# Optimization experiments

Hardware: AMD Instinct MI355X
Metric: run time of the kernel (lower is better)

The kernel has to match this reference:

```python
import jax, jax.numpy as jnp
import numpy as np

N, IN_DIM, HEADS, C = 100000, 128, 4, 32  # out_dim = HEADS*C = 128
E = 1600000


def setup_inputs() -> dict:
    key = jax.random.key(0)
    ks = jax.random.split(key, 9)
    x = jax.random.normal(ks[0], (N, IN_DIM), dtype=jnp.float32)
    edge_index = jax.random.randint(ks[1], (2, E), 0, N, dtype=jnp.int64)
    # GATConv params
    W = jax.random.normal(ks[2], (HEADS * C, IN_DIM), dtype=jnp.float32) * (1.0 / np.sqrt(IN_DIM))
    att_src = jax.random.normal(ks[3], (HEADS, C), dtype=jnp.float32) * 0.1
    att_dst = jax.random.normal(ks[4], (HEADS, C), dtype=jnp.float32) * 0.1
    bias = jax.random.normal(ks[5], (HEADS * C,), dtype=jnp.float32) * 0.01
    # complex phase + LayerNorm params
    phase = jax.random.normal(ks[6], (HEADS * C,), dtype=jnp.float32) * 0.02
    gamma = 1.0 + jax.random.normal(ks[7], (HEADS * C,), dtype=jnp.float32) * 0.01
    beta = jax.random.normal(ks[8], (HEADS * C,), dtype=jnp.float32) * 0.01
    return {"x": x, "edge_index": edge_index, "W": W, "att_src": att_src,
            "att_dst": att_dst, "bias": bias, "phase": phase, "gamma": gamma, "beta": beta}


def reference(x, edge_index, W, att_src, att_dst, bias, phase, gamma, beta):
    src, dst = edge_index[0], edge_index[1]
    h = (x @ W.T).reshape(N, HEADS, C)                      # [N,H,C]
    a_src = jnp.einsum('nhc,hc->nh', h, att_src)            # [N,H]
    a_dst = jnp.einsum('nhc,hc->nh', h, att_dst)
    e = jax.nn.leaky_relu(a_src[src] + a_dst[dst], 0.2)     # [E,H]
    # segment softmax over destination nodes (numerically stable)
    m = jax.ops.segment_max(e, dst, num_segments=N)         # [N,H]
    ex = jnp.exp(e - m[dst])
    s = jax.ops.segment_sum(ex, dst, num_segments=N)        # [N,H]
    alpha = ex / (s[dst] + 1e-16)                           # [E,H]
    msg = h[src] * alpha[:, :, None]                        # [E,H,C]
    out = jax.ops.segment_sum(msg, dst, num_segments=N).reshape(N, HEADS * C) + bias
    # complex phase magnitude: sqrt((h cos p)^2 + (h sin p)^2 + eps)
    mag = jnp.sqrt((out * jnp.cos(phase)) ** 2 + (out * jnp.sin(phase)) ** 2 + 1e-12)
    # LayerNorm
    mu = mag.mean(-1, keepdims=True)
    var = ((mag - mu) ** 2).mean(-1, keepdims=True)
    hn = (mag - mu) / jnp.sqrt(var + 1e-5) * gamma + beta
    return jax.nn.gelu(hn, approximate=False)
```

## Files before the change

kernel.cpp:

```cpp
#include <hip/hip_runtime.h>
#include <hip/hip_bf16.h>

#define N_ 100000
#define E_ 1600000
#define D_ 128
#define H_ 4
#define C_ 32
#define CAP 64
#define XSTR 136
#define NBUILD 256
#define NLIN 512

using bf16 = __hip_bfloat16;
typedef __attribute__((ext_vector_type(8))) short short8;
typedef __attribute__((ext_vector_type(4))) float f32x4;
typedef __attribute__((ext_vector_type(2))) float f32x2;

__device__ __forceinline__ float u2f(unsigned u) { return __uint_as_float(u); }
__device__ __forceinline__ unsigned short f2bu(float v) {
  bf16 t = __float2bfloat16(v);
  return *(unsigned short*)&t;
}

__global__ __launch_bounds__(256) void k_build_linear(
    const float* __restrict__ x, const float* __restrict__ W,
    const float* __restrict__ att_src, const float* __restrict__ att_dst,
    const int* __restrict__ ei, int* __restrict__ cnt, int* __restrict__ slot,
    bf16* __restrict__ h, float* __restrict__ a_src, float* __restrict__ a_dst) {
  __shared__ unsigned short WB[16384];
  __shared__ unsigned short XS[64 * XSTR];
  __shared__ float ats[128], atd[128];
  const int tid = threadIdx.x;
  const int bid = blockIdx.x;
  const int role = bid % 3;

  if (role == 0) {
    const int bb = bid / 3;
    for (int base = bb * 1024; base < E_; base += NBUILD * 1024) {
      const int e0 = base + tid;
      const int e1 = base + 256 + tid;
      const int e2 = base + 512 + tid;
      const int e3 = base + 768 + tid;
      int d0 = 0, d1 = 0, d2 = 0, d3 = 0, s0 = 0, s1 = 0, s2 = 0, s3 = 0;
      if (e0 < E_) { d0 = ei[E_ + e0]; s0 = ei[e0]; }
      if (e1 < E_) { d1 = ei[E_ + e1]; s1 = ei[e1]; }
      if (e2 < E_) { d2 = ei[E_ + e2]; s2 = ei[e2]; }
      if (e3 < E_) { d3 = ei[E_ + e3]; s3 = ei[e3]; }
      if (e0 < E_) { const int p = atomicAdd(&cnt[d0], 1); if (p < CAP) slot[d0 * CAP + p] = s0; }
      if (e1 < E_) { const int p = atomicAdd(&cnt[d1], 1); if (p < CAP) slot[d1 * CAP + p] = s1; }
      if (e2 < E_) { const int p = atomicAdd(&cnt[d2], 1); if (p < CAP) slot[d2 * CAP + p] = s2; }
      if (e3 < E_) { const int p = atomicAdd(&cnt[d3], 1); if (p < CAP) slot[d3 * CAP + p] = s3; }
    }
    return;
  }

  const int lb = (bid / 3) * 2 + (role - 1);
  const int lane = tid & 63, w = tid >> 6;
  const int n15 = lane & 15, quad = lane >> 4;

  for (int i = tid; i < 16384; i += 256) {
    const int n = i >> 7, k = i & 127;
    const int kk = k >> 5, q = (k >> 3) & 3, j = k & 7;
    const int frag = kk * 8 + (n >> 4);
    WB[frag * 512 + q * 128 + (n & 15) * 8 + j] = f2bu(W[n * 128 + k]);
  }
  if (tid < 128) { ats[tid] = att_src[tid]; atd[tid] = att_dst[tid]; }
  __syncthreads();

  const int nrb = (N_ + 63) / 64;
  for (int rb = lb; rb < nrb; rb += NLIN) {
    const int row0 = rb * 64;
    const int arow = row0 + w * 16 + n15;

    short8 af[4];
#pragma unroll
    for (int kk = 0; kk < 4; kk++) {
      float4 p = make_float4(0.f, 0.f, 0.f, 0.f);
      float4 q = make_float4(0.f, 0.f, 0.f, 0.f);
      if (arow < N_) {
        const float* xp = &x[(size_t)arow * 128 + kk * 32 + quad * 8];
        p = *(const float4*)xp;
        q = *(const float4*)(xp + 4);
      }
      short8 a;
      a[0] = f2bu(p.x); a[1] = f2bu(p.y); a[2] = f2bu(p.z); a[3] = f2bu(p.w);
      a[4] = f2bu(q.x); a[5] = f2bu(q.y); a[6] = f2bu(q.z); a[7] = f2bu(q.w);
      af[kk] = a;
    }

    f32x4 acc[8] = {};
#pragma unroll
    for (int kk = 0; kk < 4; kk++)
#pragma unroll
      for (int t = 0; t < 8; t++) {
        const short8 b = *(const short8*)&WB[(kk * 8 + t) * 512 + lane * 8];
        acc[t] = __builtin_amdgcn_mfma_f32_16x16x32_bf16(af[kk], b, acc[t], 0, 0, 0);
      }

#pragma unroll
    for (int t = 0; t < 8; t++)
#pragma unroll
      for (int reg = 0; reg < 4; reg++)
        XS[(w * 16 + quad * 4 + reg) * XSTR + t * 16 + n15] = f2bu(acc[t][reg]);

    const int lrow = lane >> 2, hd = lane & 3, cb = hd * 32;
    const int grow = row0 + w * 16 + lrow;
    if (grow < N_) {
      float ps = 0.f, pd = 0.f;
#pragma unroll
      for (int g = 0; g < 4; g++) {
        const uint4 v = *(const uint4*)&XS[(w * 16 + lrow) * XSTR + cb + g * 8];
        *(uint4*)&h[(size_t)grow * 128 + cb + g * 8] = v;
        const unsigned uu[4] = {v.x, v.y, v.z, v.w};
#pragma unroll
        for (int p2 = 0; p2 < 4; p2++) {
          const float f0 = u2f(uu[p2] << 16);
          const float f1 = u2f(uu[p2] & 0xffff0000u);
          const int cc = cb + g * 8 + p2 * 2;
          ps = fmaf(f0, ats[cc], ps);  ps = fmaf(f1, ats[cc + 1], ps);
          pd = fmaf(f0, atd[cc], pd);  pd = fmaf(f1, atd[cc + 1], pd);
        }
      }
      a_src[grow * 4 + hd] = ps;
      a_dst[grow * 4 + hd] = pd;
    }
  }
}

__global__ __launch_bounds__(256) void k_gather(
    const int* __restrict__ cnt, const int* __restrict__ slot,
    const float* __restrict__ a_src, const float* __restrict__ a_dst,
    const bf16* __restrict__ h, const float* __restrict__ bias,
    const float* __restrict__ gamma, const float* __restrict__ beta,
    float* __restrict__ out) {
  const int lane = threadIdx.x & 63;
  const int d = blockIdx.x * 4 + (threadIdx.x >> 6);
  if (d >= N_) return;
  const int head = lane >> 4;
  const int ch = lane * 2;
  const int deg0 = cnt[d];
  const int deg = deg0 < CAP ? deg0 : CAP;
  const float ad = a_dst[d * 4 + head];
  const int* __restrict__ srow = slot + (size_t)d * CAP;

  int my_src = 0;
  if (lane < deg) my_src = srow[lane];

  float acc0 = 0.f, acc1 = 0.f, sumw = 0.f;

  int j = 0;
  for (; j + 4 <= deg; j += 4) {
    const int s0 = __builtin_amdgcn_readlane(my_src, j);
    const int s1 = __builtin_amdgcn_readlane(my_src, j + 1);
    const int s2 = __builtin_amdgcn_readlane(my_src, j + 2);
    const int s3 = __builtin_amdgcn_readlane(my_src, j + 3);
    const float as0 = a_src[s0 * 4 + head];
    const float as1 = a_src[s1 * 4 + head];
    const float as2 = a_src[s2 * 4 + head];
    const float as3 = a_src[s3 * 4 + head];
    const unsigned h0 = *(const unsigned*)&h[((size_t)s0 << 7) + ch];
    const unsigned h1 = *(const unsigned*)&h[((size_t)s1 << 7) + ch];
    const unsigned h2 = *(const unsigned*)&h[((size_t)s2 << 7) + ch];
    const unsigned h3 = *(const unsigned*)&h[((size_t)s3 << 7) + ch];
    float e0 = as0 + ad; e0 = (e0 > 0.f) ? e0 : 0.2f * e0;
    float e1 = as1 + ad; e1 = (e1 > 0.f) ? e1 : 0.2f * e1;
    float e2 = as2 + ad; e2 = (e2 > 0.f) ? e2 : 0.2f * e2;
    float e3 = as3 + ad; e3 = (e3 > 0.f) ? e3 : 0.2f * e3;
    const float w0 = __expf(e0), w1 = __expf(e1);
    const float w2 = __expf(e2), w3 = __expf(e3);
    sumw += w0; sumw += w1; sumw += w2; sumw += w3;
    acc0 = fmaf(w0, u2f(h0 << 16), acc0); acc1 = fmaf(w0, u2f(h0 & 0xffff0000u), acc1);
    acc0 = fmaf(w1, u2f(h1 << 16), acc0); acc1 = fmaf(w1, u2f(h1 & 0xffff0000u), acc1);
    acc0 = fmaf(w2, u2f(h2 << 16), acc0); acc1 = fmaf(w2, u2f(h2 & 0xffff0000u), acc1);
    acc0 = fmaf(w3, u2f(h3 << 16), acc0); acc1 = fmaf(w3, u2f(h3 & 0xffff0000u), acc1);
  }
  for (; j < deg; ++j) {
    const int s = __builtin_amdgcn_readlane(my_src, j);
    const float as = a_src[s * 4 + head];
    const unsigned hv = *(const unsigned*)&h[((size_t)s << 7) + ch];
    float ev = as + ad;
    ev = (ev > 0.f) ? ev : 0.2f * ev;
    const float wv = __expf(ev);
    sumw += wv;
    acc0 = fmaf(wv, u2f(hv << 16), acc0);
    acc1 = fmaf(wv, u2f(hv & 0xffff0000u), acc1);
  }

  const float inv = 1.0f / (sumw + 1e-16f);
  const float2 bi = *(const float2*)&bias[ch];
  const float v0 = acc0 * inv + bi.x;
  const float v1 = acc1 * inv + bi.y;
  const float m0i = sqrtf(v0 * v0 + 1e-12f);
  const float m1i = sqrtf(v1 * v1 + 1e-12f);

  float s1r = m0i + m1i;
#pragma unroll
  for (int off = 32; off > 0; off >>= 1) s1r += __shfl_xor(s1r, off);
  const float mu = s1r * (1.0f / 128.0f);
  const float d0 = m0i - mu, d1 = m1i - mu;
  float q = d0 * d0 + d1 * d1;
#pragma unroll
  for (int off = 32; off > 0; off >>= 1) q += __shfl_xor(q, off);
  const float rstd = rsqrtf(q * (1.0f / 128.0f) + 1e-5f);
  const float2 ga = *(const float2*)&gamma[ch];
  const float2 be = *(const float2*)&beta[ch];
  const float hn0 = d0 * rstd * ga.x + be.x;
  const float hn1 = d1 * rstd * ga.y + be.y;
  const float g0 = 0.5f * hn0 * (1.0f + erff(hn0 * 0.70710678118654752f));
  const float g1 = 0.5f * hn1 * (1.0f + erff(hn1 * 0.70710678118654752f));
  f32x2 gv; gv.x = g0; gv.y = g1;
  __builtin_nontemporal_store(gv, (f32x2*)&out[(size_t)d * 128 + ch]);
}

extern "C" void kernel_launch(void* const* d_in, const int* in_sizes, int n_in,
                              void* d_out, int out_size, void* d_ws, size_t ws_size,
                              hipStream_t stream) {
  const float* x       = (const float*)d_in[0];
  const int*   ei      = (const int*)d_in[1];
  const float* W       = (const float*)d_in[2];
  const float* att_src = (const float*)d_in[3];
  const float* att_dst = (const float*)d_in[4];
  const float* bias    = (const float*)d_in[5];
  const float* gamma   = (const float*)d_in[7];
  const float* beta    = (const float*)d_in[8];
  float* out = (float*)d_out;

  bf16*  h     = (bf16*)d_ws;
  float* a_src = (float*)(h + (size_t)N_ * D_);
  float* a_dst = a_src + (size_t)N_ * H_;
  int*   cnt   = (int*)(a_dst + (size_t)N_ * H_);
  int*   slot  = cnt + (size_t)N_;

  (void)hipMemsetAsync(cnt, 0, (size_t)N_ * sizeof(int), stream);

  k_build_linear<<<768, 256, 0, stream>>>(x, W, att_src, att_dst, ei, cnt,
                                          slot, h, a_src, a_dst);
  k_gather<<<(N_ + 3) / 4, 256, 0, stream>>>(cnt, slot, a_src, a_dst, h,
                                             bias, gamma, beta, out);
}
```

Measured before the change: 289.7 us.

## Process four edges per wave iteration using 16-byte row loads in gather

The gather kernel now splits each wave into four 16-lane groups. Each group handles a different neighbor edge and loads 8 bf16 channels per lane with one 16-byte load, instead of every lane walking all edges one at a time with 4-byte loads. Partial accumulators are then combined with cross-group shuffles and staged through shared memory to return to the per-lane 2-channel layout for the LayerNorm/GELU epilogue. This cuts serial loop iterations and the number of memory instructions per edge, at the cost of extra shuffles and an LDS round-trip. The LDS write and read within the wave have no explicit barrier, so correctness relies on wave-level execution.

```diff
diff --git a/kernel.cpp b/kernel.cpp
--- a/kernel.cpp
+++ b/kernel.cpp
@@ -133,65 +133,64 @@
     const bf16* __restrict__ h, const float* __restrict__ bias,
     const float* __restrict__ gamma, const float* __restrict__ beta,
     float* __restrict__ out) {
-  const int lane = threadIdx.x & 63;
-  const int d = blockIdx.x * 4 + (threadIdx.x >> 6);
+  __shared__ float RED[4][128];
+  const int tid = threadIdx.x;
+  const int lane = tid & 63;
+  const int wid = tid >> 6;
+  const int d = blockIdx.x * 4 + wid;
   if (d >= N_) return;
-  const int head = lane >> 4;
-  const int ch = lane * 2;
+  const int g = lane >> 4;
+  const int l16 = lane & 15;
+  const int headp = l16 >> 2;
+  const int ch0 = l16 * 8;
   const int deg0 = cnt[d];
   const int deg = deg0 < CAP ? deg0 : CAP;
-  const float ad = a_dst[d * 4 + head];
+  const float ad = a_dst[d * 4 + headp];
   const int* __restrict__ srow = slot + (size_t)d * CAP;
 
   int my_src = 0;
   if (lane < deg) my_src = srow[lane];
 
-  float acc0 = 0.f, acc1 = 0.f, sumw = 0.f;
-
-  int j = 0;
-  for (; j + 4 <= deg; j += 4) {
-    const int s0 = __builtin_amdgcn_readlane(my_src, j);
-    const int s1 = __builtin_amdgcn_readlane(my_src, j + 1);
-    const int s2 = __builtin_amdgcn_readlane(my_src, j + 2);
-    const int s3 = __builtin_amdgcn_readlane(my_src, j + 3);
-    const float as0 = a_src[s0 * 4 + head];
-    const float as1 = a_src[s1 * 4 + head];
-    const float as2 = a_src[s2 * 4 + head];
-    const float as3 = a_src[s3 * 4 + head];
-    const unsigned h0 = *(const unsigned*)&h[((size_t)s0 << 7) + ch];
-    const unsigned h1 = *(const unsigned*)&h[((size_t)s1 << 7) + ch];
-    const unsigned h2 = *(const unsigned*)&h[((size_t)s2 << 7) + ch];
-    const unsigned h3 = *(const unsigned*)&h[((size_t)s3 << 7) + ch];
-    float e0 = as0 + ad; e0 = (e0 > 0.f) ? e0 : 0.2f * e0;
-    float e1 = as1 + ad; e1 = (e1 > 0.f) ? e1 : 0.2f * e1;
-    float e2 = as2 + ad; e2 = (e2 > 0.f) ? e2 : 0.2f * e2;
-    float e3 = as3 + ad; e3 = (e3 > 0.f) ? e3 : 0.2f * e3;
-    const float w0 = __expf(e0), w1 = __expf(e1);
-    const float w2 = __expf(e2), w3 = __expf(e3);
-    sumw += w0; sumw += w1; sumw += w2; sumw += w3;
-    acc0 = fmaf(w0, u2f(h0 << 16), acc0); acc1 = fmaf(w0, u2f(h0 & 0xffff0000u), acc1);
-    acc0 = fmaf(w1, u2f(h1 << 16), acc0); acc1 = fmaf(w1, u2f(h1 & 0xffff0000u), acc1);
-    acc0 = fmaf(w2, u2f(h2 << 16), acc0); acc1 = fmaf(w2, u2f(h2 & 0xffff0000u), acc1);
-    acc0 = fmaf(w3, u2f(h3 << 16), acc0); acc1 = fmaf(w3, u2f(h3 & 0xffff0000u), acc1);
-  }
-  for (; j < deg; ++j) {
-    const int s = __builtin_amdgcn_readlane(my_src, j);
-    const float as = a_src[s * 4 + head];
-    const unsigned hv = *(const unsigned*)&h[((size_t)s << 7) + ch];
-    float ev = as + ad;
+  float acc[8] = {0.f, 0.f, 0.f, 0.f, 0.f, 0.f, 0.f, 0.f};
+  float sumw = 0.f;
+
+  for (int base = 0; base < deg; base += 4) {
+    const int idx = base + g;
+    const bool live = idx < deg;
+    const int s = __shfl(my_src, live ? idx : 0);
+    float ev = a_src[s * 4 + headp] + ad;
     ev = (ev > 0.f) ? ev : 0.2f * ev;
-    const float wv = __expf(ev);
-    sumw += wv;
-    acc0 = fmaf(wv, u2f(hv << 16), acc0);
-    acc1 = fmaf(wv, u2f(hv & 0xffff0000u), acc1);
-  }
+    const float w = live ? __expf(ev) : 0.f;
+    sumw += w;
+    const uint4 hv = *(const uint4*)&h[((size_t)s << 7) + ch0];
+    const unsigned uu[4] = {hv.x, hv.y, hv.z, hv.w};
+#pragma unroll
+    for (int p = 0; p < 4; p++) {
+      acc[p * 2]     = fmaf(w, u2f(uu[p] << 16), acc[p * 2]);
+      acc[p * 2 + 1] = fmaf(w, u2f(uu[p] & 0xffff0000u), acc[p * 2 + 1]);
+    }
+  }
+
+#pragma unroll
+  for (int p = 0; p < 8; p++) {
+    acc[p] += __shfl_xor(acc[p], 16);
+    acc[p] += __shfl_xor(acc[p], 32);
+  }
+  sumw += __shfl_xor(sumw, 16);
+  sumw += __shfl_xor(sumw, 32);
 
   const float inv = 1.0f / (sumw + 1e-16f);
-  const float2 bi = *(const float2*)&bias[ch];
-  const float v0 = acc0 * inv + bi.x;
-  const float v1 = acc1 * inv + bi.y;
-  const float m0i = sqrtf(v0 * v0 + 1e-12f);
-  const float m1i = sqrtf(v1 * v1 + 1e-12f);
+  if (g == 0) {
+    const float4 b0 = *(const float4*)&bias[ch0];
+    const float4 b1 = *(const float4*)&bias[ch0 + 4];
+    const float bb[8] = {b0.x, b0.y, b0.z, b0.w, b1.x, b1.y, b1.z, b1.w};
+#pragma unroll
+    for (int p = 0; p < 8; p++) RED[wid][ch0 + p] = acc[p] * inv + bb[p];
+  }
+  const int ch = lane * 2;
+  const float2 vv = *(const float2*)&RED[wid][ch];
+  const float m0i = sqrtf(vv.x * vv.x + 1e-12f);
+  const float m1i = sqrtf(vv.y * vv.y + 1e-12f);
 
   float s1r = m0i + m1i;
 #pragma unroll
```

Result: slower. 298.7 us (+3.1%).
